# Kernel tuning notes

Measured on AMD Instinct MI355X. Metric: run time of the kernel, lower is better.

The kernel has to match this reference:

```python
import jax, jax.numpy as jnp
import numpy as np

B, S, D, E = 8, 4096, 1024, 3
EPS = 1e-5


def setup_inputs() -> dict:
    key = jax.random.key(0)
    ks = jax.random.split(key, 4)
    s = 0.02  # init scale for weights
    return {
        "inputs": jax.random.normal(ks[0], (B, S, D), jnp.float32),
        "current_state": jnp.zeros((B, D), jnp.float32),
        "norm_w": jnp.ones((D,), jnp.float32),              # RMSNorm weight
        "router_w": jax.random.normal(ks[1], (D, E), jnp.float32) * s,
        "router_b": jnp.zeros((E,), jnp.float32),
        "w_gh": jax.random.normal(ks[2], (E, D, 2 * D), jnp.float32) * s,  # per-expert minGRU hidden+gate proj
        "w_out": jax.random.normal(ks[3], (E, D, D), jnp.float32) * s,     # per-expert proj_out
    }


def _rmsnorm(x, w, eps=EPS):
    return x * jax.lax.rsqrt(jnp.mean(x * x, axis=-1, keepdims=True) + eps) * w


def _g(x):
    # minGRU continuous activation g(x) = x + 0.5 for x >= 0 else sigmoid(x)
    return jnp.where(x >= 0, x + 0.5, jax.nn.sigmoid(x))


def reference(inputs, current_state, norm_w, router_w, router_b, w_gh, w_out):
    x = _rmsnorm(inputs, norm_w)                       # [B,S,D]
    # SMEAR: route per sample (mean-pooled features), soft-merge expert weights
    logits = jnp.mean(x, axis=1) @ router_w + router_b  # [B,E]
    probs = jax.nn.softmax(logits, axis=-1)             # [B,E]
    Wg = jnp.einsum('be,eij->bij', probs, w_gh)         # [B,D,2D] merged gate/hidden weights
    Wo = jnp.einsum('be,eij->bij', probs, w_out)        # [B,D,D]  merged output proj
    hg = jnp.einsum('bsi,bij->bsj', x, Wg)              # [B,S,2D]
    hid, gate = jnp.split(hg, 2, axis=-1)
    z = jax.nn.sigmoid(gate)                            # update gate
    a = 1.0 - z                                         # decay coefficient
    b = z * _g(hid)                                     # input term
    # fold initial state into first step: h_0 contribution
    b = b.at[:, 0].add(a[:, 0] * current_state)
    # linear recurrence h_t = a_t * h_{t-1} + b_t via associative scan over time
    def comb(c1, c2):
        a1, b1 = c1
        a2, b2 = c2
        return a1 * a2, a2 * b1 + b2
    _, h = jax.lax.associative_scan(comb, (a, b), axis=1)  # [B,S,D]
    new_state = h[:, -1]
    out = jnp.einsum('bsi,bij->bsj', h, Wo) + inputs       # proj_out + residual
    aux_loss = jnp.float32(0.0)
    return out, new_state, aux_loss
```

## Files before the change

### kernel.cpp

```cpp
#include <hip/hip_runtime.h>
#include <hip/hip_bf16.h>
#include <cstdint>
#include <cstddef>

using bf16 = __bf16;
typedef __bf16 bf16x8 __attribute__((ext_vector_type(8)));
typedef __bf16 bf16x4 __attribute__((ext_vector_type(4)));
typedef float  f32x4  __attribute__((ext_vector_type(4)));

#define DEV __device__ __forceinline__

DEV float sigmoidf_(float x) { return 1.0f / (1.0f + __expf(-x)); }

typedef __attribute__((address_space(1))) void as1_void;
typedef __attribute__((address_space(3))) void as3_void;

DEV void load16_lds(const void* g, void* l) {
  __builtin_amdgcn_global_load_lds((as1_void*)(void*)g, (as3_void*)l, 16, 0, 0);
}

__global__ __launch_bounds__(256) void k_rms_x(const float* __restrict__ inp,
                                               const float* __restrict__ nw,
                                               bf16* __restrict__ x) {
  const int row = blockIdx.x;
  const int t = threadIdx.x;
  const float* r = inp + (size_t)row * 1024 + t * 4;
  f32x4 v = *(const f32x4*)r;
  float ss = v[0]*v[0] + v[1]*v[1] + v[2]*v[2] + v[3]*v[3];
  __shared__ float red[4];
  for (int off = 32; off; off >>= 1) ss += __shfl_down(ss, off);
  if ((t & 63) == 0) red[t >> 6] = ss;
  __syncthreads();
  float tot = red[0] + red[1] + red[2] + red[3];
  float sc = rsqrtf(tot * (1.0f / 1024.0f) + 1e-5f);
  f32x4 w = *(const f32x4*)(nw + t * 4);
  bf16x4 o;
  o[0] = (bf16)(v[0] * sc * w[0]); o[1] = (bf16)(v[1] * sc * w[1]);
  o[2] = (bf16)(v[2] * sc * w[2]); o[3] = (bf16)(v[3] * sc * w[3]);
  *(bf16x4*)(x + (size_t)row * 1024 + t * 4) = o;
}

__global__ __launch_bounds__(256) void k_colsum(const bf16* __restrict__ x,
                                                float* __restrict__ part) {
  const int b = blockIdx.y, c = blockIdx.x;
  const int d = threadIdx.x * 4;
  f32x4 s = {0.f, 0.f, 0.f, 0.f};
  const bf16* base = x + ((size_t)b * 4096 + (size_t)c * 128) * 1024 + d;
  for (int i = 0; i < 128; ++i) {
    bf16x4 v = *(const bf16x4*)(base + (size_t)i * 1024);
    s[0] += (float)v[0]; s[1] += (float)v[1];
    s[2] += (float)v[2]; s[3] += (float)v[3];
  }
  *(f32x4*)(part + ((size_t)(b * 32 + c)) * 1024 + d) = s;
}

__global__ __launch_bounds__(256) void k_router(const float* __restrict__ part,
                                                const float* __restrict__ rw,
                                                const float* __restrict__ rb,
                                                float* __restrict__ probs,
                                                float* __restrict__ aux) {
  const int b = blockIdx.x;
  const int t = threadIdx.x;
  __shared__ float red[4];
  __shared__ float lg[3];
  f32x4 cs = {0.f, 0.f, 0.f, 0.f};
  #pragma unroll 8
  for (int c = 0; c < 32; ++c)
    cs += *(const f32x4*)(part + ((size_t)(b * 32 + c)) * 1024 + t * 4);
  for (int e = 0; e < 3; ++e) {
    float dot = cs[0] * rw[(t*4+0)*3+e] + cs[1] * rw[(t*4+1)*3+e]
              + cs[2] * rw[(t*4+2)*3+e] + cs[3] * rw[(t*4+3)*3+e];
    for (int off = 32; off; off >>= 1) dot += __shfl_down(dot, off);
    if ((t & 63) == 0) red[t >> 6] = dot;
    __syncthreads();
    if (t == 0) lg[e] = (red[0]+red[1]+red[2]+red[3]) * (1.0f/4096.0f) + rb[e];
    __syncthreads();
  }
  if (t == 0) {
    float m = fmaxf(lg[0], fmaxf(lg[1], lg[2]));
    float p0 = __expf(lg[0]-m), p1 = __expf(lg[1]-m), p2 = __expf(lg[2]-m);
    float inv = 1.0f / (p0 + p1 + p2);
    probs[b*3+0] = p0*inv; probs[b*3+1] = p1*inv; probs[b*3+2] = p2*inv;
    if (b == 0) *aux = 0.0f;
  }
}

__global__ __launch_bounds__(256) void k_mixT(const float* __restrict__ W,
                                              const float* __restrict__ probs,
                                              bf16* __restrict__ out,
                                              int Ncols) {
  const int b = blockIdx.z;
  const int i0 = blockIdx.y * 64;
  const int j0 = blockIdx.x * 64;
  const float p0 = probs[b*3+0], p1 = probs[b*3+1], p2 = probs[b*3+2];
  __shared__ float tile[64][68];
  const int t = threadIdx.x;
  const int jl = (t & 15) * 4;
  const size_t estr = (size_t)1024 * Ncols;
  for (int ii = 0; ii < 4; ++ii) {
    int il = (t >> 4) + ii * 16;
    const float* src = W + (size_t)(i0 + il) * Ncols + (j0 + jl);
    f32x4 v0 = *(const f32x4*)(src);
    f32x4 v1 = *(const f32x4*)(src + estr);
    f32x4 v2 = *(const f32x4*)(src + 2 * estr);
    f32x4 v = p0 * v0 + p1 * v1 + p2 * v2;
    tile[il][jl+0] = v[0]; tile[il][jl+1] = v[1];
    tile[il][jl+2] = v[2]; tile[il][jl+3] = v[3];
  }
  __syncthreads();
  bf16* ob = out + (size_t)b * Ncols * 1024;
  const int il2 = (t & 15) * 4;
  for (int jj = 0; jj < 4; ++jj) {
    int jl2 = (t >> 4) + jj * 16;
    bf16x4 o;
    o[0] = (bf16)tile[il2+0][jl2]; o[1] = (bf16)tile[il2+1][jl2];
    o[2] = (bf16)tile[il2+2][jl2]; o[3] = (bf16)tile[il2+3][jl2];
    *(bf16x4*)(ob + (size_t)(j0 + jl2) * 1024 + (i0 + il2)) = o;
  }
}

template<int EPI>
__global__ __launch_bounds__(256) void k_gemm(const bf16* __restrict__ A,
                                              const bf16* __restrict__ Bt,
                                              const float* __restrict__ addend,
                                              float* __restrict__ Cout,
                                              bf16* __restrict__ pa,
                                              bf16* __restrict__ pb,
                                              int M, int N, int K) {
  const int bz = blockIdx.z;
  const int tm = blockIdx.y, tn = blockIdx.x;
  __shared__ __align__(16) char smem[32768];
  bf16* sA = (bf16*)smem;
  bf16* sB = (bf16*)(smem + 16384);
  const int tid = threadIdx.x;
  const int lane = tid & 63, w = tid >> 6;
  const int wm = (w >> 1) * 64, wn = (w & 1) * 64;
  const int l15 = lane & 15, quad = lane >> 4;
  const bf16* Ab  = A + (size_t)bz * M * K + (size_t)tm * 128 * K;
  const bf16* Btb = Bt + (size_t)bz * N * K;
  f32x4 acc[4][4] = {};

  for (int k0 = 0; k0 < K; k0 += 64) {
    #pragma unroll
    for (int i = 0; i < 4; ++i) {
      const int q   = i * 256 + w * 64 + lane;
      const int row = q >> 3;
      const int kc  = (q & 7) ^ (row & 7);
      load16_lds(Ab + (size_t)row * K + k0 + kc * 8, (char*)sA + q * 16);
      int nrow;
      if constexpr (EPI == 0) {
        const int c = row;
        const int jloc = tn * 64 + (c >> 6) * 32 + (c & 31);
        nrow = jloc + (((c & 63) >= 32) ? 1024 : 0);
      } else {
        nrow = tn * 128 + row;
      }
      load16_lds(Btb + (size_t)nrow * K + k0 + kc * 8, (char*)sB + q * 16);
    }
    __syncthreads();
    #pragma unroll
    for (int ks = 0; ks < 2; ++ks) {
      bf16x8 af[4], bfr[4];
      const int kc = ks * 4 + quad;
      #pragma unroll
      for (int mi = 0; mi < 4; ++mi) {
        int m = wm + mi * 16 + l15;
        af[mi] = *(const bf16x8*)(sA + (size_t)(m * 8 + (kc ^ (m & 7))) * 8);
      }
      #pragma unroll
      for (int ni = 0; ni < 4; ++ni) {
        int n = wn + ni * 16 + l15;
        bfr[ni] = *(const bf16x8*)(sB + (size_t)(n * 8 + (kc ^ (n & 7))) * 8);
      }
      #pragma unroll
      for (int mi = 0; mi < 4; ++mi)
        #pragma unroll
        for (int ni = 0; ni < 4; ++ni)
          acc[mi][ni] = __builtin_amdgcn_mfma_f32_16x16x32_bf16(
              af[mi], bfr[ni], acc[mi][ni], 0, 0, 0);
    }
    __syncthreads();
  }

  if constexpr (EPI == 0) {
    bf16* Aab = pa + (size_t)bz * M * 1024;
    bf16* Bab = pb + (size_t)bz * M * 1024;
    const int jbase = tn * 64 + (wn >> 1);
    #pragma unroll
    for (int mi = 0; mi < 4; ++mi)
      #pragma unroll
      for (int ni = 0; ni < 2; ++ni)
        #pragma unroll
        for (int r = 0; r < 4; ++r) {
          int srow = tm * 128 + wm + mi * 16 + quad * 4 + r;
          float hid = acc[mi][ni][r];
          float gt  = acc[mi][ni + 2][r];
          float z = sigmoidf_(gt);
          float av = 1.0f - z;
          float gv = (hid >= 0.0f) ? (hid + 0.5f) : sigmoidf_(hid);
          float bv = z * gv;
          size_t oidx = (size_t)srow * 1024 + jbase + ni * 16 + l15;
          Aab[oidx] = (bf16)av;
          Bab[oidx] = (bf16)bv;
        }
  } else {
    float* sC = (float*)smem;
    const int ST = 132;
    float* C = Cout + (size_t)bz * M * N;
    const float* Ain = addend + (size_t)bz * M * N;
    #pragma unroll
    for (int p = 0; p < 4; ++p) {
      __syncthreads();
      if ((wm >> 6) == (p >> 1)) {
        const int m0 = (p & 1) * 2;
        #pragma unroll
        for (int mi = m0; mi < m0 + 2; ++mi)
          #pragma unroll
          for (int ni = 0; ni < 4; ++ni)
            #pragma unroll
            for (int r = 0; r < 4; ++r) {
              int lrow = mi * 16 + quad * 4 + r - (p & 1) * 32;
              sC[lrow * ST + wn + ni * 16 + l15] = acc[mi][ni][r];
            }
      }
      __syncthreads();
      #pragma unroll
      for (int i = 0; i < 4; ++i) {
        int v = i * 256 + tid;
        int rl = v >> 5, c4 = (v & 31) * 4;
        int grow = tm * 128 + p * 32 + rl;
        int gcol = tn * 128 + c4;
        f32x4 cv = *(f32x4*)(sC + rl * ST + c4);
        f32x4 ad = *(const f32x4*)(Ain + (size_t)grow * N + gcol);
        *(f32x4*)(C + (size_t)grow * N + gcol) = cv + ad;
      }
    }
  }
}

__global__ __launch_bounds__(256) void k_scan1(const bf16* __restrict__ Aab,
                                               const bf16* __restrict__ Bab,
                                               float* __restrict__ cA,
                                               float* __restrict__ cB) {
  const int b = blockIdx.y, c = blockIdx.x;
  const int d = threadIdx.x * 4;
  f32x4 A = {1.f, 1.f, 1.f, 1.f}, Bv = {0.f, 0.f, 0.f, 0.f};
  const size_t base = ((size_t)(b * 4096 + c * 64)) * 1024 + d;
  #pragma unroll 4
  for (int i = 0; i < 64; ++i) {
    bf16x4 av = *(const bf16x4*)(Aab + base + (size_t)i * 1024);
    bf16x4 bv = *(const bf16x4*)(Bab + base + (size_t)i * 1024);
    #pragma unroll
    for (int j = 0; j < 4; ++j) {
      float a = (float)av[j], bb = (float)bv[j];
      A[j] *= a; Bv[j] = a * Bv[j] + bb;
    }
  }
  *(f32x4*)(cA + ((size_t)(b * 64 + c)) * 1024 + d) = A;
  *(f32x4*)(cB + ((size_t)(b * 64 + c)) * 1024 + d) = Bv;
}

__global__ __launch_bounds__(256) void k_scan2(const float* __restrict__ cA,
                                               const float* __restrict__ cB,
                                               const float* __restrict__ state,
                                               float* __restrict__ hin,
                                               float* __restrict__ ns) {
  const int gid = blockIdx.x * 256 + threadIdx.x;
  const int b = gid >> 10, d = gid & 1023;
  float h = state[gid];
  for (int c0 = 0; c0 < 64; c0 += 8) {
    float ar[8], br[8];
    #pragma unroll
    for (int i = 0; i < 8; ++i) {
      size_t idx = (((size_t)(b * 64 + c0 + i)) << 10) + d;
      ar[i] = cA[idx]; br[i] = cB[idx];
    }
    #pragma unroll
    for (int i = 0; i < 8; ++i) {
      size_t idx = (((size_t)(b * 64 + c0 + i)) << 10) + d;
      hin[idx] = h;
      h = ar[i] * h + br[i];
    }
  }
  ns[gid] = h;
}

__global__ __launch_bounds__(256) void k_scan3(const bf16* __restrict__ Aab,
                                               const bf16* __restrict__ Bab,
                                               const float* __restrict__ hin,
                                               bf16* __restrict__ hq) {
  const int b = blockIdx.y, c = blockIdx.x;
  const int d = threadIdx.x * 4;
  f32x4 h = *(const f32x4*)(hin + ((size_t)(b * 64 + c)) * 1024 + d);
  const size_t base = ((size_t)(b * 4096 + c * 64)) * 1024 + d;
  bf16* ob = hq + base;
  #pragma unroll 4
  for (int i = 0; i < 64; ++i) {
    bf16x4 av = *(const bf16x4*)(Aab + base + (size_t)i * 1024);
    bf16x4 bv = *(const bf16x4*)(Bab + base + (size_t)i * 1024);
    bf16x4 o;
    #pragma unroll
    for (int j = 0; j < 4; ++j) {
      h[j] = (float)av[j] * h[j] + (float)bv[j];
      o[j] = (bf16)h[j];
    }
    *(bf16x4*)(ob + (size_t)i * 1024) = o;
  }
}

extern "C" void kernel_launch(void* const* d_in, const int* in_sizes, int n_in,
                              void* d_out, int out_size, void* d_ws, size_t ws_size,
                              hipStream_t stream) {
  const float* inputs   = (const float*)d_in[0];
  const float* state    = (const float*)d_in[1];
  const float* norm_w   = (const float*)d_in[2];
  const float* router_w = (const float*)d_in[3];
  const float* router_b = (const float*)d_in[4];
  const float* w_gh     = (const float*)d_in[5];
  const float* w_out    = (const float*)d_in[6];

  float* out = (float*)d_out;
  float* new_state = out + (size_t)8 * 4096 * 1024;
  float* aux = new_state + 8 * 1024;

  char* ws = (char*)d_ws;
  size_t off = 0;
  auto alloc = [&](size_t bytes) {
    char* p = ws + off;
    off = (off + bytes + 255) & ~(size_t)255;
    return p;
  };
  bf16*  x    = (bf16*)alloc((size_t)8 * 4096 * 1024 * 2);
  bf16*  a_ar = (bf16*)alloc((size_t)8 * 4096 * 1024 * 2);
  bf16*  b_ar = (bf16*)alloc((size_t)8 * 4096 * 1024 * 2);
  bf16*  hq   = (bf16*)alloc((size_t)8 * 4096 * 1024 * 2);
  bf16*  WgT  = (bf16*)alloc((size_t)8 * 2048 * 1024 * 2);
  bf16*  WoT  = (bf16*)alloc((size_t)8 * 1024 * 1024 * 2);
  float* part = (float*)alloc((size_t)8 * 32 * 1024 * 4);
  float* probs = (float*)alloc(256);
  float* cA   = (float*)alloc((size_t)8 * 64 * 1024 * 4);
  float* cB   = (float*)alloc((size_t)8 * 64 * 1024 * 4);
  float* hin  = (float*)alloc((size_t)8 * 64 * 1024 * 4);
  (void)in_sizes; (void)n_in; (void)out_size; (void)ws_size;

  k_rms_x <<<32768, 256, 0, stream>>>(inputs, norm_w, x);
  k_colsum<<<dim3(32, 8), 256, 0, stream>>>(x, part);
  k_router<<<8, 256, 0, stream>>>(part, router_w, router_b, probs, aux);
  k_mixT  <<<dim3(32, 16, 8), 256, 0, stream>>>(w_gh, probs, WgT, 2048);
  k_mixT  <<<dim3(16, 16, 8), 256, 0, stream>>>(w_out, probs, WoT, 1024);
  k_gemm<0><<<dim3(16, 32, 8), 256, 0, stream>>>(x, WgT, nullptr, nullptr,
                                                 a_ar, b_ar, 4096, 2048, 1024);
  k_scan1 <<<dim3(64, 8), 256, 0, stream>>>(a_ar, b_ar, cA, cB);
  k_scan2 <<<32, 256, 0, stream>>>(cA, cB, state, hin, new_state);
  k_scan3 <<<dim3(64, 8), 256, 0, stream>>>(a_ar, b_ar, hin, hq);
  k_gemm<1><<<dim3(8, 32, 8), 256, 0, stream>>>(hq, WoT, inputs, out,
                                                nullptr, nullptr, 4096, 1024, 1024);
}
```

Baseline: 654.9 us.

## Use 256x256 double-buffered GEMM tiles with block swizzle for both projections

Replaces the 128x128 single-buffered GEMM with a 256x256 tile, 512-thread kernel that double-buffers LDS (128KB) so global-to-LDS loads for the next K-step overlap the MFMA work on the current one. It also remaps block indices with a swizzle to improve L2 reuse, and interleaves LDS fragment loads with MFMA groups. The aim is higher arithmetic intensity and hidden load latency, at the cost of one workgroup per CU, heavy register use from the 8x4 accumulators, and fewer blocks in flight.

```diff
diff --git a/kernel.cpp b/kernel.cpp
--- a/kernel.cpp
+++ b/kernel.cpp
@@ -120,122 +120,177 @@
 }
 
 template<int EPI>
-__global__ __launch_bounds__(256) void k_gemm(const bf16* __restrict__ A,
-                                              const bf16* __restrict__ Bt,
-                                              const float* __restrict__ addend,
-                                              float* __restrict__ Cout,
-                                              bf16* __restrict__ pa,
-                                              bf16* __restrict__ pb,
-                                              int M, int N, int K) {
+__global__ __launch_bounds__(512, 1) void k_gemm256(const bf16* __restrict__ A,
+                                                    const bf16* __restrict__ Bt,
+                                                    const float* __restrict__ addend,
+                                                    float* __restrict__ Cout,
+                                                    bf16* __restrict__ pa,
+                                                    bf16* __restrict__ pb,
+                                                    int M, int N, int K) {
   const int bz = blockIdx.z;
-  const int tm = blockIdx.y, tn = blockIdx.x;
-  __shared__ __align__(16) char smem[32768];
-  bf16* sA = (bf16*)smem;
-  bf16* sB = (bf16*)(smem + 16384);
+  const int nx = gridDim.x;
+  const int nwg = nx * gridDim.y;
+  const int orig = blockIdx.y * nx + blockIdx.x;
+  const int swz = (orig & 7) * (nwg >> 3) + (orig >> 3);
+  const int tm = swz / nx, tn = swz % nx;
+
+  __shared__ __align__(16) char smem[131072];
   const int tid = threadIdx.x;
   const int lane = tid & 63, w = tid >> 6;
-  const int wm = (w >> 1) * 64, wn = (w & 1) * 64;
   const int l15 = lane & 15, quad = lane >> 4;
-  const bf16* Ab  = A + (size_t)bz * M * K + (size_t)tm * 128 * K;
+  const int wm = (w >> 2) * 128;
+  const int wn = (w & 3) * 64;
+
+  const bf16* Ab  = A  + (size_t)bz * M * K;
   const bf16* Btb = Bt + (size_t)bz * N * K;
-  f32x4 acc[4][4] = {};
-
-  for (int k0 = 0; k0 < K; k0 += 64) {
-    #pragma unroll
-    for (int i = 0; i < 4; ++i) {
-      const int q   = i * 256 + w * 64 + lane;
-      const int row = q >> 3;
-      const int kc  = (q & 7) ^ (row & 7);
-      load16_lds(Ab + (size_t)row * K + k0 + kc * 8, (char*)sA + q * 16);
-      int nrow;
-      if constexpr (EPI == 0) {
-        const int c = row;
-        const int jloc = tn * 64 + (c >> 6) * 32 + (c & 31);
-        nrow = jloc + (((c & 63) >= 32) ? 1024 : 0);
-      } else {
-        nrow = tn * 128 + row;
+
+  const int row0 = tid >> 3,          kc0 = (tid & 7) ^ (row0 & 7);
+  const int row1 = (512 + tid) >> 3,  kc1 = (tid & 7) ^ (row1 & 7);
+
+  auto browf = [&](int c) -> int {
+    if constexpr (EPI == 0) {
+      return tn * 128 + ((c >> 6) * 32) + (c & 31) + (((c & 63) >= 32) ? 1024 : 0);
+    } else {
+      return tn * 256 + c;
+    }
+  };
+  const bf16* aS0_0 = Ab + (size_t)(tm*256 +       row0) * K + kc0 * 8;
+  const bf16* aS0_1 = Ab + (size_t)(tm*256 +       row1) * K + kc1 * 8;
+  const bf16* aS1_0 = Ab + (size_t)(tm*256 + 128 + row0) * K + kc0 * 8;
+  const bf16* aS1_1 = Ab + (size_t)(tm*256 + 128 + row1) * K + kc1 * 8;
+  const bf16* bS0_0 = Btb + (size_t)browf(row0)       * K + kc0 * 8;
+  const bf16* bS0_1 = Btb + (size_t)browf(row1)       * K + kc1 * 8;
+  const bf16* bS1_0 = Btb + (size_t)browf(128 + row0) * K + kc0 * 8;
+  const bf16* bS1_1 = Btb + (size_t)browf(128 + row1) * K + kc1 * 8;
+
+  const int ld0 = tid * 16;
+  const int ld1 = 8192 + tid * 16;
+  auto stage = [&](int buf, int u) {
+    load16_lds(aS0_0 + u*64, smem + buf*32768 + ld0);
+    load16_lds(aS0_1 + u*64, smem + buf*32768 + ld1);
+    load16_lds(aS1_0 + u*64, smem + buf*32768 + 16384 + ld0);
+    load16_lds(aS1_1 + u*64, smem + buf*32768 + 16384 + ld1);
+    load16_lds(bS0_0 + u*64, smem + 65536 + buf*32768 + ld0);
+    load16_lds(bS0_1 + u*64, smem + 65536 + buf*32768 + ld1);
+    load16_lds(bS1_0 + u*64, smem + 65536 + buf*32768 + 16384 + ld0);
+    load16_lds(bS1_1 + u*64, smem + 65536 + buf*32768 + 16384 + ld1);
+  };
+
+  f32x4 acc[8][4] = {};
+  bf16x8 a[4][2], b0[2][2], b1[2][2];
+
+  auto ldA = [&](int buf, int mq) {
+    const bf16* base = (const bf16*)(smem + buf*32768);
+    #pragma unroll
+    for (int mi = 0; mi < 4; ++mi) {
+      const int m = wm + mq*64 + mi*16 + l15;
+      #pragma unroll
+      for (int ks = 0; ks < 2; ++ks) {
+        const int kc = ks*4 + quad;
+        a[mi][ks] = *(const bf16x8*)(base + (size_t)(m*8 + (kc ^ (m & 7))) * 8);
       }
-      load16_lds(Btb + (size_t)nrow * K + k0 + kc * 8, (char*)sB + q * 16);
-    }
-    __syncthreads();
-    #pragma unroll
-    for (int ks = 0; ks < 2; ++ks) {
-      bf16x8 af[4], bfr[4];
-      const int kc = ks * 4 + quad;
+    }
+  };
+  auto ldB = [&](int buf, int nq, bf16x8 (&bb)[2][2]) {
+    const bf16* base = (const bf16*)(smem + 65536 + buf*32768);
+    #pragma unroll
+    for (int ni = 0; ni < 2; ++ni) {
+      const int n = wn + nq*32 + ni*16 + l15;
       #pragma unroll
-      for (int mi = 0; mi < 4; ++mi) {
-        int m = wm + mi * 16 + l15;
-        af[mi] = *(const bf16x8*)(sA + (size_t)(m * 8 + (kc ^ (m & 7))) * 8);
+      for (int ks = 0; ks < 2; ++ks) {
+        const int kc = ks*4 + quad;
+        bb[ni][ks] = *(const bf16x8*)(base + (size_t)(n*8 + (kc ^ (n & 7))) * 8);
       }
-      #pragma unroll
-      for (int ni = 0; ni < 4; ++ni) {
-        int n = wn + ni * 16 + l15;
-        bfr[ni] = *(const bf16x8*)(sB + (size_t)(n * 8 + (kc ^ (n & 7))) * 8);
-      }
-      #pragma unroll
-      for (int mi = 0; mi < 4; ++mi)
-        #pragma unroll
-        for (int ni = 0; ni < 4; ++ni)
-          acc[mi][ni] = __builtin_amdgcn_mfma_f32_16x16x32_bf16(
-              af[mi], bfr[ni], acc[mi][ni], 0, 0, 0);
-    }
+    }
+  };
+
+#define MMAC(MQ, NQ, BB)                                                        \
+  _Pragma("unroll")                                                             \
+  for (int mi = 0; mi < 4; ++mi) {                                              \
+    _Pragma("unroll")                                                           \
+    for (int ni = 0; ni < 2; ++ni) {                                            \
+      f32x4 c_ = acc[(MQ)*4 + mi][(NQ)*2 + ni];                                 \
+      c_ = __builtin_amdgcn_mfma_f32_16x16x32_bf16(a[mi][0], BB[ni][0], c_, 0, 0, 0); \
+      c_ = __builtin_amdgcn_mfma_f32_16x16x32_bf16(a[mi][1], BB[ni][1], c_, 0, 0, 0); \
+      acc[(MQ)*4 + mi][(NQ)*2 + ni] = c_;                                       \
+    }                                                                           \
+  }
+
+  const int NT = K >> 6;
+
+  stage(0, 0);
+  __syncthreads();
+
+  for (int t = 0; t < NT; ++t) {
+    const int buf = t & 1;
+    if (t + 1 < NT) stage(buf ^ 1, t + 1);
+    ldA(buf, 0);
+    ldB(buf, 0, b0);
+    MMAC(0, 0, b0);
+    ldB(buf, 1, b1);
+    MMAC(0, 1, b1);
+    ldA(buf, 1);
+    MMAC(1, 1, b1);
+    MMAC(1, 0, b0);
     __syncthreads();
   }
 
   if constexpr (EPI == 0) {
     bf16* Aab = pa + (size_t)bz * M * 1024;
     bf16* Bab = pb + (size_t)bz * M * 1024;
-    const int jbase = tn * 64 + (wn >> 1);
-    #pragma unroll
-    for (int mi = 0; mi < 4; ++mi)
+    const int jb = tn * 128 + (w & 3) * 32;
+    const int rb = tm * 256 + wm;
+    #pragma unroll
+    for (int mi = 0; mi < 8; ++mi)
       #pragma unroll
       for (int ni = 0; ni < 2; ++ni)
         #pragma unroll
         for (int r = 0; r < 4; ++r) {
-          int srow = tm * 128 + wm + mi * 16 + quad * 4 + r;
+          const int srow = rb + mi * 16 + quad * 4 + r;
           float hid = acc[mi][ni][r];
           float gt  = acc[mi][ni + 2][r];
           float z = sigmoidf_(gt);
           float av = 1.0f - z;
           float gv = (hid >= 0.0f) ? (hid + 0.5f) : sigmoidf_(hid);
           float bv = z * gv;
-          size_t oidx = (size_t)srow * 1024 + jbase + ni * 16 + l15;
+          size_t oidx = (size_t)srow * 1024 + jb + ni * 16 + l15;
           Aab[oidx] = (bf16)av;
           Bab[oidx] = (bf16)bv;
         }
   } else {
     float* sC = (float*)smem;
-    const int ST = 132;
+    const int ST = 260;
     float* C = Cout + (size_t)bz * M * N;
     const float* Ain = addend + (size_t)bz * M * N;
-    #pragma unroll
-    for (int p = 0; p < 4; ++p) {
-      __syncthreads();
-      if ((wm >> 6) == (p >> 1)) {
-        const int m0 = (p & 1) * 2;
+    #pragma unroll 1
+    for (int p = 0; p < 8; ++p) {
+      if ((w >> 2) == (p >> 2)) {
+        const int mi0 = (p & 3) * 2;
         #pragma unroll
-        for (int mi = m0; mi < m0 + 2; ++mi)
+        for (int mm = 0; mm < 2; ++mm)
           #pragma unroll
-          for (int ni = 0; ni < 4; ++ni)
+          for (int nt_ = 0; nt_ < 4; ++nt_)
             #pragma unroll
             for (int r = 0; r < 4; ++r) {
-              int lrow = mi * 16 + quad * 4 + r - (p & 1) * 32;
-              sC[lrow * ST + wn + ni * 16 + l15] = acc[mi][ni][r];
+              const int rl = mm * 16 + quad * 4 + r;
+              sC[rl * ST + (w & 3) * 64 + nt_ * 16 + l15] = acc[mi0 + mm][nt_][r];
             }
       }
       __syncthreads();
       #pragma unroll
       for (int i = 0; i < 4; ++i) {
-        int v = i * 256 + tid;
-        int rl = v >> 5, c4 = (v & 31) * 4;
-        int grow = tm * 128 + p * 32 + rl;
-        int gcol = tn * 128 + c4;
+        const int v = i * 512 + tid;
+        const int rl = v >> 6, c4 = (v & 63) * 4;
+        const int grow = tm * 256 + p * 32 + rl;
+        const int gcol = tn * 256 + c4;
         f32x4 cv = *(f32x4*)(sC + rl * ST + c4);
         f32x4 ad = *(const f32x4*)(Ain + (size_t)grow * N + gcol);
         *(f32x4*)(C + (size_t)grow * N + gcol) = cv + ad;
       }
-    }
-  }
+      __syncthreads();
+    }
+  }
+#undef MMAC
 }
 
 __global__ __launch_bounds__(256) void k_scan1(const bf16* __restrict__ Aab,
@@ -348,11 +403,11 @@
   k_router<<<8, 256, 0, stream>>>(part, router_w, router_b, probs, aux);
   k_mixT  <<<dim3(32, 16, 8), 256, 0, stream>>>(w_gh, probs, WgT, 2048);
   k_mixT  <<<dim3(16, 16, 8), 256, 0, stream>>>(w_out, probs, WoT, 1024);
-  k_gemm<0><<<dim3(16, 32, 8), 256, 0, stream>>>(x, WgT, nullptr, nullptr,
-                                                 a_ar, b_ar, 4096, 2048, 1024);
+  k_gemm256<0><<<dim3(8, 16, 8), 512, 0, stream>>>(x, WgT, nullptr, nullptr,
+                                                   a_ar, b_ar, 4096, 2048, 1024);
   k_scan1 <<<dim3(64, 8), 256, 0, stream>>>(a_ar, b_ar, cA, cB);
   k_scan2 <<<32, 256, 0, stream>>>(cA, cB, state, hin, new_state);
   k_scan3 <<<dim3(64, 8), 256, 0, stream>>>(a_ar, b_ar, hin, hq);
-  k_gemm<1><<<dim3(8, 32, 8), 256, 0, stream>>>(hq, WoT, inputs, out,
-                                                nullptr, nullptr, 4096, 1024, 1024);
-}
+  k_gemm256<1><<<dim3(4, 16, 8), 512, 0, stream>>>(hq, WoT, inputs, out,
+                                                   nullptr, nullptr, 4096, 1024, 1024);
+}
```

Result: slower. 1.249 ms (+90.7%).
